# Performance work log

Hardware: AMD Instinct MI355X
Metric: run time of the kernel (lower is better)

## Reference

```python
import jax, jax.numpy as jnp
import numpy as np

N_NODES = 50000
N_EDGES = 320000
IN_FEAT = 128
HIDDEN = 256
N_CLASSES = 40
BN_EPS = 1e-5


def _gcn_norm(edge_index, n_nodes):
    # Add self-loops (PyG gcn_norm default) and compute sym-normalized weights
    loops = jnp.arange(n_nodes, dtype=edge_index.dtype)
    src = jnp.concatenate([edge_index[0], loops])
    dst = jnp.concatenate([edge_index[1], loops])
    ones = jnp.ones(src.shape[0], dtype=jnp.float32)
    deg = jax.ops.segment_sum(ones, dst, num_segments=n_nodes)
    dinv = jnp.where(deg > 0, jax.lax.rsqrt(deg), 0.0)
    norm = dinv[src] * dinv[dst]  # [E+N]
    return src, dst, norm


def _gcn_conv(x, src, dst, norm, W, b, n_nodes):
    xw = x @ W                                   # [N, F_out]
    msg = norm[:, None] * xw[src]                # [E+N, F_out] gather
    out = jax.ops.segment_sum(msg, dst, num_segments=n_nodes)  # scatter-add
    return out + b


def _batchnorm(x, gamma, beta):
    mean = jnp.mean(x, axis=0)
    var = jnp.mean(jnp.square(x - mean), axis=0)  # biased, training-mode stats
    return (x - mean) * jax.lax.rsqrt(var + BN_EPS) * gamma + beta


def setup_inputs() -> dict:
    key = jax.random.key(0)
    ks = jax.random.split(key, 8)
    x = jax.random.normal(ks[0], (N_NODES, IN_FEAT), dtype=jnp.float32)
    edge_index = jax.random.randint(ks[1], (2, N_EDGES), 0, N_NODES, dtype=jnp.int64)
    s1 = 1.0 / np.sqrt(IN_FEAT)
    s2 = 1.0 / np.sqrt(HIDDEN)
    return {
        "x": x,
        "edge_index": edge_index,
        "W1": jax.random.normal(ks[2], (IN_FEAT, HIDDEN), dtype=jnp.float32) * s1,
        "b1": jnp.zeros((HIDDEN,), dtype=jnp.float32),
        "g1": jnp.ones((HIDDEN,), dtype=jnp.float32),
        "be1": jnp.zeros((HIDDEN,), dtype=jnp.float32),
        "W2": jax.random.normal(ks[3], (HIDDEN, HIDDEN), dtype=jnp.float32) * s2,
        "b2": jnp.zeros((HIDDEN,), dtype=jnp.float32),
        "g2": jnp.ones((HIDDEN,), dtype=jnp.float32),
        "be2": jnp.zeros((HIDDEN,), dtype=jnp.float32),
        "W3": jax.random.normal(ks[4], (HIDDEN, N_CLASSES), dtype=jnp.float32) * s2,
        "b3": jnp.zeros((N_CLASSES,), dtype=jnp.float32),
    }


def reference(x, edge_index, W1, b1, g1, be1, W2, b2, g2, be2, W3, b3):
    n = x.shape[0]
    src, dst, norm = _gcn_norm(edge_index, n)
    # layer 1
    h = _gcn_conv(x, src, dst, norm, W1, b1, n)
    h = jax.nn.relu(_batchnorm(h, g1, be1))
    # layer 2
    h = _gcn_conv(h, src, dst, norm, W2, b2, n)
    h = jax.nn.relu(_batchnorm(h, g2, be2))
    # output layer
    h = _gcn_conv(h, src, dst, norm, W3, b3, n)
    return jax.nn.log_softmax(h, axis=1)
```

## Files before the change

### kernel.cpp

```cpp
#include <hip/hip_runtime.h>

#define N_NODES 50000
#define N_EDGES 320000
#define IN_FEAT 128
#define HIDDEN  256
#define NCLS    40
#define BN_EPS  1e-5f

#define SCAN_B  256
#define SCAN_NB ((N_NODES + SCAN_B - 1) / SCAN_B)
#define GNB     (N_NODES / 16)
#define AGG_T   ((N_NODES + 63) / 64)

#define PREP_HIST_NB  (N_EDGES / 256)
#define PREP_CVT_NB   (N_NODES * IN_FEAT / 8 / 256)
#define PREP_PACK_NB  54
#define BNA_NB        (N_NODES * HIDDEN / 8 / 256)

typedef __attribute__((ext_vector_type(8))) _Float16 f16x8;
typedef __attribute__((ext_vector_type(2))) _Float16 f16x2;
typedef __attribute__((ext_vector_type(4))) float f32x4;

__device__ __forceinline__ f16x2 pkmax0(f16x2 a) {
    return __builtin_elementwise_max(a, (f16x2)(_Float16)0.f);
}

__device__ __forceinline__ void packB_unit(const float* __restrict__ W,
                                           _Float16* __restrict__ Bp,
                                           int nt, int kt, int nkt, int M, int lane) {
    const int n = nt * 16 + (lane & 15);
    const int kb = kt * 32 + (lane >> 4) * 8;
    _Float16* dst = Bp + (((size_t)nt * nkt + kt) * 64 + lane) * 8;
#pragma unroll
    for (int j = 0; j < 8; j++)
        dst[j] = (n < M) ? (_Float16)W[(size_t)(kb + j) * M + n] : (_Float16)0.f;
}

__global__ __launch_bounds__(256) void k_prep(const int* __restrict__ e_dst,
                                              int* __restrict__ counts,
                                              const float* __restrict__ x,
                                              _Float16* __restrict__ Xh,
                                              const float* __restrict__ W1,
                                              const float* __restrict__ W2,
                                              const float* __restrict__ W3,
                                              _Float16* __restrict__ W1p,
                                              _Float16* __restrict__ W2p,
                                              _Float16* __restrict__ W3p) {
    const int b = blockIdx.x;
    const int tid = threadIdx.x;
    if (b < PREP_HIST_NB) {
        const int e = b * 256 + tid;
        atomicAdd(&counts[e_dst[e]], 1);
    } else if (b < PREP_HIST_NB + PREP_CVT_NB) {
        const int i = (b - PREP_HIST_NB) * 256 + tid;
        float4 a = *(const float4*)(x + (size_t)i * 8);
        float4 c = *(const float4*)(x + (size_t)i * 8 + 4);
        f16x8 o = {(_Float16)a.x, (_Float16)a.y, (_Float16)a.z, (_Float16)a.w,
                   (_Float16)c.x, (_Float16)c.y, (_Float16)c.z, (_Float16)c.w};
        *(f16x8*)&Xh[(size_t)i * 8] = o;
    } else {
        const int wave = tid >> 6, lane = tid & 63;
        const int u = (b - PREP_HIST_NB - PREP_CVT_NB) * 4 + wave;
        if (u < 64) {
            packB_unit(W1, W1p, u >> 2, u & 3, 4, HIDDEN, lane);
        } else if (u < 192) {
            const int v = u - 64;
            packB_unit(W2, W2p, v >> 3, v & 7, 8, HIDDEN, lane);
        } else {
            const int v = u - 192;
            packB_unit(W3, W3p, v >> 3, v & 7, 8, NCLS, lane);
        }
    }
}

__global__ __launch_bounds__(SCAN_B) void k_scan_local(const int* __restrict__ counts,
                                                       int* __restrict__ rowp,
                                                       int* __restrict__ partials) {
    __shared__ int s[SCAN_B];
    const int tid = threadIdx.x;
    const int i = blockIdx.x * SCAN_B + tid;
    int v = (i < N_NODES) ? counts[i] : 0;
    s[tid] = v;
    __syncthreads();
    for (int off = 1; off < SCAN_B; off <<= 1) {
        int t = (tid >= off) ? s[tid - off] : 0;
        __syncthreads();
        s[tid] += t;
        __syncthreads();
    }
    if (i < N_NODES) rowp[i] = s[tid] - v;
    if (tid == SCAN_B - 1) partials[blockIdx.x] = s[SCAN_B - 1];
}

__global__ __launch_bounds__(SCAN_B) void k_scan_add(int* __restrict__ rowp,
                                                     int* __restrict__ cursor,
                                                     const int* __restrict__ partials,
                                                     const int* __restrict__ counts,
                                                     float* __restrict__ dinv) {
    __shared__ int s[SCAN_B];
    const int tid = threadIdx.x;
    const int b = blockIdx.x;
    int v = (tid < b) ? partials[tid] : 0;
    s[tid] = v;
    __syncthreads();
    for (int off = SCAN_B / 2; off > 0; off >>= 1) {
        if (tid < off) s[tid] += s[tid + off];
        __syncthreads();
    }
    const int offset = s[0];
    const int i = b * SCAN_B + tid;
    if (i < N_NODES) {
        int r = rowp[i] + offset;
        rowp[i] = r;
        cursor[i] = r;
        dinv[i] = rsqrtf(1.0f + (float)counts[i]);
    }
    if (b == 0 && tid == 0) rowp[N_NODES] = N_EDGES;
}

__global__ void k_scatter(const int* __restrict__ src, const int* __restrict__ dst,
                          int* __restrict__ cursor, const float* __restrict__ dinv,
                          int2* __restrict__ edat) {
    int e = blockIdx.x * blockDim.x + threadIdx.x;
    if (e < N_EDGES) {
        int d = dst[e], s = src[e];
        int p = atomicAdd(&cursor[d], 1);
        int2 v; v.x = s; v.y = __float_as_int(dinv[s] * dinv[d]);
        edat[p] = v;
    }
}

template <int KIN>
__global__ __launch_bounds__(256, 4) void k_agg(const _Float16* __restrict__ Xin,
                                                const int* __restrict__ rowp,
                                                const int2* __restrict__ edat,
                                                const float* __restrict__ dinv,
                                                _Float16* __restrict__ Hagg) {
    constexpr int NCH = KIN / 32;
    constexpr int RW8 = KIN / 8;
    const int chunk = blockIdx.x % NCH;
    const int tile  = blockIdx.x / NCH;
    const int lane = threadIdx.x & 63;
    const int wave = threadIdx.x >> 6;
    const int sub  = lane >> 2;
    const int t    = lane & 3;
    const int sb   = lane & 60;
    int node = tile * 64 + wave * 16 + sub;
    const bool valid = node < N_NODES;
    if (!valid) node = N_NODES - 1;
    const int e0 = rowp[node];
    const int deg = valid ? (rowp[node + 1] - e0) : 0;

    int pidx[4]; float pw[4];
#pragma unroll
    for (int k = 0; k < 4; k++) {
        const int j = t + 4 * k;
        pidx[k] = node; pw[k] = 0.f;
        if (j < deg) {
            const int2 e = edat[e0 + j];
            pidx[k] = e.x; pw[k] = __int_as_float(e.y);
        }
    }
    const int wi = chunk * 4 + t;
    const float dd = dinv[node];
    const f16x2 sw2 = (f16x2)(_Float16)(dd * dd);
    const f16x8* __restrict__ Xr = (const f16x8*)Xin;
    union U8 { f16x8 v; f16x2 h[4]; };

    U8 a;
    {
        U8 r; r.v = Xr[(size_t)node * RW8 + wi];
#pragma unroll
        for (int p = 0; p < 4; p++) a.h[p] = sw2 * r.h[p];
    }
    auto batch8 = [&](int j0) {
        int bi[8]; _Float16 bw[8];
#pragma unroll
        for (int j = 0; j < 8; j++) {
            const int jj = j0 + j;
            const int   v  = __shfl(pidx[jj >> 2], sb + (jj & 3));
            const float wv = __shfl(pw[jj >> 2],  sb + (jj & 3));
            const bool ok = jj < deg;
            bi[j] = ok ? v : node;
            bw[j] = ok ? (_Float16)wv : (_Float16)0.f;
        }
        U8 r[8];
#pragma unroll
        for (int j = 0; j < 8; j++) r[j].v = Xr[(size_t)bi[j] * RW8 + wi];
        __builtin_amdgcn_sched_barrier(0);
#pragma unroll
        for (int j = 0; j < 8; j++) {
            const f16x2 w2 = (f16x2)bw[j];
#pragma unroll
            for (int p = 0; p < 4; p++) a.h[p] = w2 * r[j].h[p] + a.h[p];
        }
    };
    batch8(0);
    if (__any(deg > 8)) {
        batch8(8);
        if (__any(deg > 16)) {
            for (int j = 16; j < deg; j++) {
                const int2 ed = edat[e0 + j];
                const f16x2 w2 = (f16x2)(_Float16)__int_as_float(ed.y);
                U8 r; r.v = Xr[(size_t)ed.x * RW8 + wi];
#pragma unroll
                for (int p = 0; p < 4; p++) a.h[p] = w2 * r.h[p] + a.h[p];
            }
        }
    }
    if (valid) *(f16x8*)&Hagg[(size_t)node * KIN + wi * 8] = a.v;
}

template <int KIN>
__global__ __launch_bounds__(256, 4) void k_gemm(const _Float16* __restrict__ Hagg,
                                                 const _Float16* __restrict__ Bp,
                                                 const float* __restrict__ bias,
                                                 _Float16* __restrict__ C,
                                                 float* __restrict__ bnp2) {
    constexpr int nkt = KIN / 32;
    constexpr int LROW = KIN + 8;
    constexpr int RW8 = KIN / 8;
    __shared__ __align__(16) _Float16 At[16 * LROW];
    const int tid = threadIdx.x;
    const int rowb = blockIdx.x * 16;
#pragma unroll
    for (int it = 0; it < (16 * RW8) / 256; it++) {
        const int w = it * 256 + tid;
        const int rr = w / RW8, cw = w % RW8;
        *(f16x8*)&At[rr * LROW + cw * 8] =
            ((const f16x8*)Hagg)[(size_t)rowb * RW8 + w];
    }
    __syncthreads();

    const int wave = threadIdx.x >> 6;
    const int lane = threadIdx.x & 63;
    const int ntile0 = wave * 4;
    const _Float16* aL = &At[(lane & 15) * LROW + (lane >> 4) * 8];
    f32x4 acc[4] = {};
#pragma unroll
    for (int kt = 0; kt < nkt; kt++) {
        f16x8 af = *(const f16x8*)(aL + kt * 32);
#pragma unroll
        for (int nt = 0; nt < 4; nt++) {
            f16x8 bfr = *(const f16x8*)(Bp + (((size_t)(ntile0 + nt) * nkt + kt) * 64 + lane) * 8);
            acc[nt] = __builtin_amdgcn_mfma_f32_16x16x32_f16(af, bfr, acc[nt], 0, 0, 0);
        }
    }
    const int rg = lane >> 4, cc = lane & 15;
    float s[4], q2[4];
#pragma unroll
    for (int nt = 0; nt < 4; nt++) {
        const int col = (ntile0 + nt) * 16 + cc;
        const float b = bias[col];
        f32x4 a2 = acc[nt];
        a2[0] += b; a2[1] += b; a2[2] += b; a2[3] += b;
        const size_t base = (size_t)(rowb + rg * 4) * HIDDEN + col;
#pragma unroll
        for (int i = 0; i < 4; i++) C[base + (size_t)i * HIDDEN] = (_Float16)a2[i];
        s[nt] = a2[0] + a2[1] + a2[2] + a2[3];
        q2[nt] = a2[0]*a2[0] + a2[1]*a2[1] + a2[2]*a2[2] + a2[3]*a2[3];
    }
#pragma unroll
    for (int nt = 0; nt < 4; nt++) {
        s[nt] += __shfl_xor(s[nt], 16); s[nt] += __shfl_xor(s[nt], 32);
        q2[nt] += __shfl_xor(q2[nt], 16); q2[nt] += __shfl_xor(q2[nt], 32);
    }
    if (lane < 16) {
        float* dst = bnp2 + ((blockIdx.x & 31) * 512) + ntile0 * 16 + lane;
#pragma unroll
        for (int nt = 0; nt < 4; nt++) {
            atomicAdd(&dst[nt * 16], s[nt]);
            atomicAdd(&dst[nt * 16 + 256], q2[nt]);
        }
    }
}

__global__ __launch_bounds__(256) void k_bnprep(const float* __restrict__ bnp2,
                                                const float* __restrict__ g,
                                                const float* __restrict__ be,
                                                float* __restrict__ scale,
                                                float* __restrict__ shift) {
    const int f = threadIdx.x;
    float s = 0.f, q = 0.f;
#pragma unroll
    for (int b = 0; b < 32; b++) {
        s += bnp2[(size_t)b * 512 + f];
        q += bnp2[(size_t)b * 512 + 256 + f];
    }
    const float inv_n = 1.0f / (float)N_NODES;
    float mean = s * inv_n;
    float var = q * inv_n - mean * mean;
    var = fmaxf(var, 0.f);
    float sc = g[f] * rsqrtf(var + BN_EPS);
    scale[f] = sc;
    shift[f] = be[f] - mean * sc;
}

__global__ __launch_bounds__(256) void k_bnapply(_Float16* __restrict__ H,
                                                 const float* __restrict__ scale,
                                                 const float* __restrict__ shift) {
    const size_t i = (size_t)blockIdx.x * 256 + threadIdx.x;
    const int f0 = (int)(i & 31) * 8;
    union U8 { f16x8 v; f16x2 h[4]; } r;
    r.v = ((const f16x8*)H)[i];
#pragma unroll
    for (int p = 0; p < 4; p++) {
        f16x2 sc = {(_Float16)scale[f0 + 2 * p], (_Float16)scale[f0 + 2 * p + 1]};
        f16x2 sh = {(_Float16)shift[f0 + 2 * p], (_Float16)shift[f0 + 2 * p + 1]};
        r.h[p] = pkmax0(sc * r.h[p] + sh);
    }
    ((f16x8*)H)[i] = r.v;
}

template <int K_>
__global__ __launch_bounds__(64) void k_gemm3(const _Float16* __restrict__ A,
                                              const _Float16* __restrict__ Bp,
                                              const float* __restrict__ scale,
                                              const float* __restrict__ shift,
                                              _Float16* __restrict__ C) {
    constexpr int nkt = K_ / 32;
    constexpr int MT = 3;
    const int lane = threadIdx.x & 63;
    const int rowb = blockIdx.x * 16;
    const int koff = (lane >> 4) * 8;
    const _Float16* aptr = A + (size_t)(rowb + (lane & 15)) * K_ + koff;
    f32x4 acc[MT] = {};
#pragma unroll
    for (int kt = 0; kt < nkt; kt++) {
        union { f16x8 v; f16x2 h[4]; } au, tu;
        au.v = *(const f16x8*)(aptr + kt * 32);
        const int kb = kt * 32 + koff;
#pragma unroll
        for (int p = 0; p < 4; p++) {
            f16x2 sc2 = {(_Float16)scale[kb + 2 * p], (_Float16)scale[kb + 2 * p + 1]};
            f16x2 sh2 = {(_Float16)shift[kb + 2 * p], (_Float16)shift[kb + 2 * p + 1]};
            tu.h[p] = pkmax0(sc2 * au.h[p] + sh2);
        }
#pragma unroll
        for (int nt = 0; nt < MT; nt++) {
            f16x8 bfr = *(const f16x8*)(Bp + (((size_t)nt * nkt + kt) * 64 + lane) * 8);
            acc[nt] = __builtin_amdgcn_mfma_f32_16x16x32_f16(tu.v, bfr, acc[nt], 0, 0, 0);
        }
    }
    const int rg = lane >> 4, cc = lane & 15;
#pragma unroll
    for (int nt = 0; nt < MT; nt++) {
        const int col = nt * 16 + cc;
        if (col < NCLS) {
            const size_t base = (size_t)(rowb + rg * 4) * NCLS + col;
#pragma unroll
            for (int i = 0; i < 4; i++) C[base + (size_t)i * NCLS] = (_Float16)acc[nt][i];
        }
    }
}

__global__ __launch_bounds__(256) void k_out(const _Float16* __restrict__ XW,
                                             const int* __restrict__ rowp,
                                             const int2* __restrict__ edat,
                                             const float* __restrict__ dinv,
                                             const float* __restrict__ bias,
                                             float* __restrict__ out) {
    const int wave = threadIdx.x >> 6;
    const int lane = threadIdx.x & 63;
    const int node = blockIdx.x * 4 + wave;
    const float dd = dinv[node];
    const bool act = lane < NCLS;
    const int e0 = rowp[node];
    const int deg = rowp[node + 1] - e0;
    int pidx = 0; float pw = 0.f;
    if (lane < deg) {
        const int2 e = edat[e0 + lane];
        pidx = e.x; pw = __int_as_float(e.y);
    }
    const _Float16* Xl = XW + lane;
    float acc = 0.f;
    if (act) acc = dd * dd * (float)Xl[(size_t)node * NCLS];
    auto batch8 = [&](int j0) {
        int bi[8]; float bw[8];
#pragma unroll
        for (int j = 0; j < 8; j++) {
            const int   v  = __shfl(pidx, j0 + j);
            const float wv = __shfl(pw,  j0 + j);
            const bool ok = (j0 + j) < deg;
            bi[j] = ok ? v : node;
            bw[j] = ok ? wv : 0.f;
        }
        if (act) {
            float rv[8];
#pragma unroll
            for (int j = 0; j < 8; j++) rv[j] = (float)Xl[(size_t)bi[j] * NCLS];
            __builtin_amdgcn_sched_barrier(0);
#pragma unroll
            for (int j = 0; j < 8; j++) acc += bw[j] * rv[j];
        }
    };
    batch8(0);
    if (deg > 8) {
        batch8(8);
        if (deg > 16) {
            batch8(16);
            if (deg > 24) {
                batch8(24);
                if (deg > 32) {
                    for (int j = 32; j < deg; j++) {
                        const int2 ed = edat[e0 + j];
                        if (act) acc += __int_as_float(ed.y) * (float)Xl[(size_t)ed.x * NCLS];
                    }
                }
            }
        }
    }
    if (act) acc += bias[lane];
    float m = act ? acc : -1e30f;
#pragma unroll
    for (int off = 32; off > 0; off >>= 1) m = fmaxf(m, __shfl_xor(m, off));
    float e = act ? expf(acc - m) : 0.f;
#pragma unroll
    for (int off = 32; off > 0; off >>= 1) e += __shfl_xor(e, off);
    const float lse = m + logf(e);
    if (act) out[node * NCLS + lane] = acc - lse;
}

extern "C" void kernel_launch(void* const* d_in, const int* in_sizes, int n_in,
                              void* d_out, int out_size, void* d_ws, size_t ws_size,
                              hipStream_t stream) {
    const float* x   = (const float*)d_in[0];
    const int*   ei  = (const int*)d_in[1];
    const float* W1  = (const float*)d_in[2];
    const float* b1  = (const float*)d_in[3];
    const float* g1  = (const float*)d_in[4];
    const float* be1 = (const float*)d_in[5];
    const float* W2  = (const float*)d_in[6];
    const float* b2  = (const float*)d_in[7];
    const float* g2  = (const float*)d_in[8];
    const float* be2 = (const float*)d_in[9];
    const float* W3  = (const float*)d_in[10];
    const float* b3  = (const float*)d_in[11];
    float* out = (float*)d_out;

    const int* e_src = ei;
    const int* e_dst = ei + N_EDGES;

    char* w = (char*)d_ws;
    _Float16* Xh  = (_Float16*)w;              w += (size_t)N_NODES * IN_FEAT * 2;
    _Float16* H1h = (_Float16*)w;              w += (size_t)N_NODES * HIDDEN * 2;
    _Float16* H2h = (_Float16*)w;              w += (size_t)N_NODES * HIDDEN * 2;
    _Float16* Sagg = (_Float16*)w;             w += (size_t)N_NODES * HIDDEN * 2;
    _Float16* XW3h = (_Float16*)w;             w += (size_t)N_NODES * NCLS * 2;
    float* dinv   = (float*)w;                 w += (size_t)N_NODES * 4;
    int2*  edat   = (int2*)w;                  w += (size_t)N_EDGES * 8;
    int*   counts = (int*)w;                   w += (size_t)N_NODES * 4;
    float* bnp2a  = (float*)w;                 w += (size_t)32 * 512 * 4;
    float* bnp2b  = (float*)w;                 w += (size_t)32 * 512 * 4;
    int*   rowp   = (int*)w;                   w += (size_t)(N_NODES + 4) * 4;
    int*   cursor = (int*)w;                   w += (size_t)N_NODES * 4;
    int*   partials=(int*)w;                   w += 256 * 4;
    float* scale1 = (float*)w;                 w += 256 * 4;
    float* shift1 = (float*)w;                 w += 256 * 4;
    float* scale2 = (float*)w;                 w += 256 * 4;
    float* shift2 = (float*)w;                 w += 256 * 4;
    _Float16* W1p = (_Float16*)w;              w += (size_t)16 * 4 * 64 * 8 * 2;
    _Float16* W2p = (_Float16*)w;              w += (size_t)16 * 8 * 64 * 8 * 2;
    _Float16* W3p = (_Float16*)w;              w += (size_t)3 * 8 * 64 * 8 * 2;

    const int EB = (N_EDGES + 255) / 256;

    hipMemsetAsync(counts, 0, (size_t)N_NODES * 4 + 2 * (size_t)32 * 512 * 4, stream);
    k_prep<<<PREP_HIST_NB + PREP_CVT_NB + PREP_PACK_NB, 256, 0, stream>>>(
        e_dst, counts, x, Xh, W1, W2, W3, W1p, W2p, W3p);
    k_scan_local<<<SCAN_NB, SCAN_B, 0, stream>>>(counts, rowp, partials);
    k_scan_add<<<SCAN_NB, SCAN_B, 0, stream>>>(rowp, cursor, partials, counts, dinv);
    k_scatter<<<EB, 256, 0, stream>>>(e_src, e_dst, cursor, dinv, edat);

    k_agg<IN_FEAT><<<AGG_T * (IN_FEAT / 32), 256, 0, stream>>>(
        Xh, rowp, edat, dinv, Sagg);
    k_gemm<IN_FEAT><<<GNB, 256, 0, stream>>>(Sagg, W1p, b1, H1h, bnp2a);
    k_bnprep<<<1, 256, 0, stream>>>(bnp2a, g1, be1, scale1, shift1);
    k_bnapply<<<BNA_NB, 256, 0, stream>>>(H1h, scale1, shift1);

    k_agg<HIDDEN><<<AGG_T * (HIDDEN / 32), 256, 0, stream>>>(
        H1h, rowp, edat, dinv, Sagg);
    k_gemm<HIDDEN><<<GNB, 256, 0, stream>>>(Sagg, W2p, b2, H2h, bnp2b);
    k_bnprep<<<1, 256, 0, stream>>>(bnp2b, g2, be2, scale2, shift2);

    k_gemm3<HIDDEN><<<GNB, 64, 0, stream>>>(H2h, W3p, scale2, shift2, XW3h);
    k_out<<<N_NODES / 4, 256, 0, stream>>>(XW3h, rowp, edat, dinv, b3, out);
}
```

Baseline: 282.8 us.

## Split neighbor aggregation by source-node half and sum partials inside GEMM

The CSR scatter now places edges from low-half sources at the front of each row and high-half sources at the back. The aggregation kernel runs separately per source half, so each pass gathers from only half of the feature matrix, which should improve L2/MALL locality. Each pass writes its own partial aggregate buffer with nontemporal stores. The following GEMM loads both partials and feeds both through MFMA, accumulating A0·W + A1·W. This doubles the aggregate write/read traffic and the MFMA work in exchange for better gather locality.

```diff
diff --git a/kernel.cpp b/kernel.cpp
--- a/kernel.cpp
+++ b/kernel.cpp
@@ -6,11 +6,12 @@
 #define HIDDEN  256
 #define NCLS    40
 #define BN_EPS  1e-5f
+#define HALFN   (N_NODES / 2)
 
 #define SCAN_B  256
 #define SCAN_NB ((N_NODES + SCAN_B - 1) / SCAN_B)
 #define GNB     (N_NODES / 16)
-#define AGG_T   ((N_NODES + 63) / 64)
+#define AGGS_T  ((N_NODES + 31) / 32)
 
 #define PREP_HIST_NB  (N_EDGES / 256)
 #define PREP_CVT_NB   (N_NODES * IN_FEAT / 8 / 256)
@@ -93,7 +94,8 @@
 }
 
 __global__ __launch_bounds__(SCAN_B) void k_scan_add(int* __restrict__ rowp,
-                                                     int* __restrict__ cursor,
+                                                     int* __restrict__ cursF,
+                                                     int* __restrict__ cursB,
                                                      const int* __restrict__ partials,
                                                      const int* __restrict__ counts,
                                                      float* __restrict__ dinv) {
@@ -112,77 +114,81 @@
     if (i < N_NODES) {
         int r = rowp[i] + offset;
         rowp[i] = r;
-        cursor[i] = r;
+        cursF[i] = r;
+        cursB[i] = r + counts[i];
         dinv[i] = rsqrtf(1.0f + (float)counts[i]);
     }
     if (b == 0 && tid == 0) rowp[N_NODES] = N_EDGES;
 }
 
 __global__ void k_scatter(const int* __restrict__ src, const int* __restrict__ dst,
-                          int* __restrict__ cursor, const float* __restrict__ dinv,
+                          int* __restrict__ cursF, int* __restrict__ cursB,
+                          const float* __restrict__ dinv,
                           int2* __restrict__ edat) {
     int e = blockIdx.x * blockDim.x + threadIdx.x;
     if (e < N_EDGES) {
         int d = dst[e], s = src[e];
-        int p = atomicAdd(&cursor[d], 1);
+        int p;
+        if (s < HALFN) p = atomicAdd(&cursF[d], 1);
+        else           p = atomicSub(&cursB[d], 1) - 1;
         int2 v; v.x = s; v.y = __float_as_int(dinv[s] * dinv[d]);
         edat[p] = v;
     }
 }
 
-template <int KIN>
-__global__ __launch_bounds__(256, 4) void k_agg(const _Float16* __restrict__ Xin,
-                                                const int* __restrict__ rowp,
-                                                const int2* __restrict__ edat,
-                                                const float* __restrict__ dinv,
-                                                _Float16* __restrict__ Hagg) {
-    constexpr int NCH = KIN / 32;
+template <int KIN, int U>
+__global__ __launch_bounds__(256, 4) void k_aggs(const _Float16* __restrict__ Xin,
+                                                 const int* __restrict__ rowp,
+                                                 const int* __restrict__ mid,
+                                                 const int2* __restrict__ edat,
+                                                 const float* __restrict__ dinv,
+                                                 _Float16* __restrict__ Hp) {
     constexpr int RW8 = KIN / 8;
-    const int chunk = blockIdx.x % NCH;
-    const int tile  = blockIdx.x / NCH;
+    const int unit = blockIdx.x % U;
+    const int tile = blockIdx.x / U;
+    const int c = unit >> 1;
+    const int h = unit & 1;
+    const int hbase = h * HALFN;
     const int lane = threadIdx.x & 63;
     const int wave = threadIdx.x >> 6;
-    const int sub  = lane >> 2;
-    const int t    = lane & 3;
-    const int sb   = lane & 60;
-    int node = tile * 64 + wave * 16 + sub;
+    const int sub  = lane >> 3;
+    const int t    = lane & 7;
+    const int sb   = lane & 56;
+    int node = tile * 32 + wave * 8 + sub;
     const bool valid = node < N_NODES;
     if (!valid) node = N_NODES - 1;
+
     const int e0 = rowp[node];
-    const int deg = valid ? (rowp[node + 1] - e0) : 0;
-
-    int pidx[4]; float pw[4];
-#pragma unroll
-    for (int k = 0; k < 4; k++) {
-        const int j = t + 4 * k;
-        pidx[k] = node; pw[k] = 0.f;
-        if (j < deg) {
-            const int2 e = edat[e0 + j];
-            pidx[k] = e.x; pw[k] = __int_as_float(e.y);
-        }
-    }
-    const int wi = chunk * 4 + t;
+    const int e1 = rowp[node + 1];
+    const int m  = mid[node];
+    const int hs = h ? m : e0;
+    int degh = h ? (e1 - m) : (m - e0);
+    if (!valid) degh = 0;
+
+    int pidx = hbase; float pw = 0.f;
+    if (t < degh) {
+        const int2 e = edat[hs + t];
+        pidx = e.x; pw = __int_as_float(e.y);
+    }
+    const int wi = c * 8 + t;
     const float dd = dinv[node];
-    const f16x2 sw2 = (f16x2)(_Float16)(dd * dd);
+    const bool selfh = ((unsigned)(node - hbase) < HALFN) && valid;
+    const f16x2 sw2 = (f16x2)(_Float16)(selfh ? dd * dd : 0.f);
     const f16x8* __restrict__ Xr = (const f16x8*)Xin;
     union U8 { f16x8 v; f16x2 h[4]; };
 
     U8 a;
     {
-        U8 r; r.v = Xr[(size_t)node * RW8 + wi];
+        U8 r; r.v = Xr[(size_t)(selfh ? node : hbase) * RW8 + wi];
 #pragma unroll
         for (int p = 0; p < 4; p++) a.h[p] = sw2 * r.h[p];
     }
-    auto batch8 = [&](int j0) {
+    {
         int bi[8]; _Float16 bw[8];
 #pragma unroll
         for (int j = 0; j < 8; j++) {
-            const int jj = j0 + j;
-            const int   v  = __shfl(pidx[jj >> 2], sb + (jj & 3));
-            const float wv = __shfl(pw[jj >> 2],  sb + (jj & 3));
-            const bool ok = jj < deg;
-            bi[j] = ok ? v : node;
-            bw[j] = ok ? (_Float16)wv : (_Float16)0.f;
+            bi[j] = __shfl(pidx, sb + j);
+            bw[j] = (_Float16)__shfl(pw, sb + j);
         }
         U8 r[8];
 #pragma unroll
@@ -194,41 +200,43 @@
 #pragma unroll
             for (int p = 0; p < 4; p++) a.h[p] = w2 * r[j].h[p] + a.h[p];
         }
-    };
-    batch8(0);
-    if (__any(deg > 8)) {
-        batch8(8);
-        if (__any(deg > 16)) {
-            for (int j = 16; j < deg; j++) {
-                const int2 ed = edat[e0 + j];
-                const f16x2 w2 = (f16x2)(_Float16)__int_as_float(ed.y);
-                U8 r; r.v = Xr[(size_t)ed.x * RW8 + wi];
-#pragma unroll
-                for (int p = 0; p < 4; p++) a.h[p] = w2 * r.h[p] + a.h[p];
-            }
-        }
-    }
-    if (valid) *(f16x8*)&Hagg[(size_t)node * KIN + wi * 8] = a.v;
+    }
+    if (__any(degh > 8)) {
+        for (int j = 8; j < degh; j++) {
+            const int2 ed = edat[hs + j];
+            const f16x2 w2 = (f16x2)(_Float16)__int_as_float(ed.y);
+            U8 r; r.v = Xr[(size_t)ed.x * RW8 + wi];
+#pragma unroll
+            for (int p = 0; p < 4; p++) a.h[p] = w2 * r.h[p] + a.h[p];
+        }
+    }
+    if (valid) {
+        _Float16* dst = Hp + (size_t)h * N_NODES * KIN + (size_t)node * KIN + wi * 8;
+        __builtin_nontemporal_store(a.v, (f16x8*)dst);
+    }
 }
 
 template <int KIN>
-__global__ __launch_bounds__(256, 4) void k_gemm(const _Float16* __restrict__ Hagg,
-                                                 const _Float16* __restrict__ Bp,
-                                                 const float* __restrict__ bias,
-                                                 _Float16* __restrict__ C,
-                                                 float* __restrict__ bnp2) {
+__global__ __launch_bounds__(256, 4) void k_gemmP(const _Float16* __restrict__ Hp,
+                                                  const _Float16* __restrict__ Bp,
+                                                  const float* __restrict__ bias,
+                                                  _Float16* __restrict__ C,
+                                                  float* __restrict__ bnp2) {
     constexpr int nkt = KIN / 32;
     constexpr int LROW = KIN + 8;
     constexpr int RW8 = KIN / 8;
-    __shared__ __align__(16) _Float16 At[16 * LROW];
+    __shared__ __align__(16) _Float16 At[2 * 16 * LROW];
     const int tid = threadIdx.x;
     const int rowb = blockIdx.x * 16;
 #pragma unroll
-    for (int it = 0; it < (16 * RW8) / 256; it++) {
-        const int w = it * 256 + tid;
-        const int rr = w / RW8, cw = w % RW8;
-        *(f16x8*)&At[rr * LROW + cw * 8] =
-            ((const f16x8*)Hagg)[(size_t)rowb * RW8 + w];
+    for (int s = 0; s < 2; s++) {
+        const f16x8* src = (const f16x8*)(Hp + (size_t)s * N_NODES * KIN);
+#pragma unroll
+        for (int it = 0; it < (16 * RW8) / 256; it++) {
+            const int w = it * 256 + tid;
+            const int rr = w / RW8, cw = w % RW8;
+            *(f16x8*)&At[(s * 16 + rr) * LROW + cw * 8] = src[(size_t)rowb * RW8 + w];
+        }
     }
     __syncthreads();
 
@@ -239,11 +247,13 @@
     f32x4 acc[4] = {};
 #pragma unroll
     for (int kt = 0; kt < nkt; kt++) {
-        f16x8 af = *(const f16x8*)(aL + kt * 32);
+        f16x8 af0 = *(const f16x8*)(aL + kt * 32);
+        f16x8 af1 = *(const f16x8*)(aL + 16 * LROW + kt * 32);
 #pragma unroll
         for (int nt = 0; nt < 4; nt++) {
             f16x8 bfr = *(const f16x8*)(Bp + (((size_t)(ntile0 + nt) * nkt + kt) * 64 + lane) * 8);
-            acc[nt] = __builtin_amdgcn_mfma_f32_16x16x32_f16(af, bfr, acc[nt], 0, 0, 0);
+            acc[nt] = __builtin_amdgcn_mfma_f32_16x16x32_f16(af0, bfr, acc[nt], 0, 0, 0);
+            acc[nt] = __builtin_amdgcn_mfma_f32_16x16x32_f16(af1, bfr, acc[nt], 0, 0, 0);
         }
     }
     const int rg = lane >> 4, cc = lane & 15;
@@ -445,7 +455,7 @@
     _Float16* Xh  = (_Float16*)w;              w += (size_t)N_NODES * IN_FEAT * 2;
     _Float16* H1h = (_Float16*)w;              w += (size_t)N_NODES * HIDDEN * 2;
     _Float16* H2h = (_Float16*)w;              w += (size_t)N_NODES * HIDDEN * 2;
-    _Float16* Sagg = (_Float16*)w;             w += (size_t)N_NODES * HIDDEN * 2;
+    _Float16* Hpool = (_Float16*)w;            w += (size_t)2 * N_NODES * HIDDEN * 2;
     _Float16* XW3h = (_Float16*)w;             w += (size_t)N_NODES * NCLS * 2;
     float* dinv   = (float*)w;                 w += (size_t)N_NODES * 4;
     int2*  edat   = (int2*)w;                  w += (size_t)N_EDGES * 8;
@@ -453,7 +463,8 @@
     float* bnp2a  = (float*)w;                 w += (size_t)32 * 512 * 4;
     float* bnp2b  = (float*)w;                 w += (size_t)32 * 512 * 4;
     int*   rowp   = (int*)w;                   w += (size_t)(N_NODES + 4) * 4;
-    int*   cursor = (int*)w;                   w += (size_t)N_NODES * 4;
+    int*   cursF  = (int*)w;                   w += (size_t)N_NODES * 4;
+    int*   cursB  = (int*)w;                   w += (size_t)N_NODES * 4;
     int*   partials=(int*)w;                   w += 256 * 4;
     float* scale1 = (float*)w;                 w += 256 * 4;
     float* shift1 = (float*)w;                 w += 256 * 4;
@@ -469,18 +480,18 @@
     k_prep<<<PREP_HIST_NB + PREP_CVT_NB + PREP_PACK_NB, 256, 0, stream>>>(
         e_dst, counts, x, Xh, W1, W2, W3, W1p, W2p, W3p);
     k_scan_local<<<SCAN_NB, SCAN_B, 0, stream>>>(counts, rowp, partials);
-    k_scan_add<<<SCAN_NB, SCAN_B, 0, stream>>>(rowp, cursor, partials, counts, dinv);
-    k_scatter<<<EB, 256, 0, stream>>>(e_src, e_dst, cursor, dinv, edat);
-
-    k_agg<IN_FEAT><<<AGG_T * (IN_FEAT / 32), 256, 0, stream>>>(
-        Xh, rowp, edat, dinv, Sagg);
-    k_gemm<IN_FEAT><<<GNB, 256, 0, stream>>>(Sagg, W1p, b1, H1h, bnp2a);
+    k_scan_add<<<SCAN_NB, SCAN_B, 0, stream>>>(rowp, cursF, cursB, partials, counts, dinv);
+    k_scatter<<<EB, 256, 0, stream>>>(e_src, e_dst, cursF, cursB, dinv, edat);
+
+    k_aggs<IN_FEAT, 4><<<AGGS_T * 4, 256, 0, stream>>>(
+        Xh, rowp, cursF, edat, dinv, Hpool);
+    k_gemmP<IN_FEAT><<<GNB, 256, 0, stream>>>(Hpool, W1p, b1, H1h, bnp2a);
     k_bnprep<<<1, 256, 0, stream>>>(bnp2a, g1, be1, scale1, shift1);
     k_bnapply<<<BNA_NB, 256, 0, stream>>>(H1h, scale1, shift1);
 
-    k_agg<HIDDEN><<<AGG_T * (HIDDEN / 32), 256, 0, stream>>>(
-        H1h, rowp, edat, dinv, Sagg);
-    k_gemm<HIDDEN><<<GNB, 256, 0, stream>>>(Sagg, W2p, b2, H2h, bnp2b);
+    k_aggs<HIDDEN, 8><<<AGGS_T * 8, 256, 0, stream>>>(
+        H1h, rowp, cursF, edat, dinv, Hpool);
+    k_gemmP<HIDDEN><<<GNB, 256, 0, stream>>>(Hpool, W2p, b2, H2h, bnp2b);
     k_bnprep<<<1, 256, 0, stream>>>(bnp2b, g2, be2, scale2, shift2);
 
     k_gemm3<HIDDEN><<<GNB, 64, 0, stream>>>(H2h, W3p, scale2, shift2, XW3h);
```

Measured after the change: 271.1 us. 1.04x faster.
